# Kernel tuning notes

Hardware: AMD Instinct MI355X
Metric: run time of the kernel (lower is better)

Reference implementation:

```python
import jax, jax.numpy as jnp
import numpy as np

SEQ, BATCH, IN_DIM, HID, OUT = 512, 256, 300, 256, 2


def setup_inputs() -> dict:
    key = jax.random.key(0)
    ks = jax.random.split(key, 7)
    s_ih = 1.0 / np.sqrt(HID)
    return {
        "x": jax.random.normal(ks[0], (SEQ, BATCH, IN_DIM), jnp.float32),
        "W_ih": jax.random.uniform(ks[1], (HID, IN_DIM), jnp.float32, -s_ih, s_ih),
        "W_hh": jax.random.uniform(ks[2], (HID, HID), jnp.float32, -s_ih, s_ih),
        "b_ih": jax.random.uniform(ks[3], (HID,), jnp.float32, -s_ih, s_ih),
        "b_hh": jax.random.uniform(ks[4], (HID,), jnp.float32, -s_ih, s_ih),
        "W_fc": jax.random.uniform(ks[5], (OUT, HID), jnp.float32, -s_ih, s_ih),
        "b_fc": jax.random.uniform(ks[6], (OUT,), jnp.float32, -s_ih, s_ih),
    }


def reference(x, W_ih, W_hh, b_ih, b_hh, W_fc, b_fc):
    # Precompute input projection for all timesteps at once: [T, B, H]
    xp = jnp.einsum('tbi,hi->tbh', x, W_ih) + b_ih + b_hh

    def step(h, xt):
        h_new = jnp.tanh(xt + h @ W_hh.T)
        return h_new, None

    h0 = jnp.zeros((x.shape[1], W_hh.shape[0]), x.dtype)
    hT, _ = jax.lax.scan(step, h0, xp)  # hT: [B, H]
    # Dropout(0.3) is identity in eval mode.
    logits = hT @ W_fc.T + b_fc  # [B, 2]
    return jax.nn.log_softmax(logits, axis=-1)
```

## Files before the change

### kernel.cpp

```cpp
#include <hip/hip_runtime.h>
#include <hip/hip_bf16.h>
#include <cstdint>
#include <cstddef>

#define SEQ 512
#define BATCH 256
#define IN_DIM 300
#define HID 256

typedef __attribute__((ext_vector_type(8))) short bf16x8;
typedef __attribute__((ext_vector_type(4))) float f32x4;

__device__ __forceinline__ unsigned short f2bf(float f) {
  union { float f; unsigned int u; } v; v.f = f;
  unsigned int u = v.u;
  return (unsigned short)((u + 0x7fffu + ((u >> 16) & 1u)) >> 16);
}
__device__ __forceinline__ unsigned short f2bf_fast(float f) {
  union { float f; unsigned int u; } v; v.f = f;
  return (unsigned short)((v.u + 0x8000u) >> 16);
}
__device__ __forceinline__ float bitsf(unsigned int u) {
  union { unsigned int u; float f; } v; v.u = u; return v.f;
}
__device__ __forceinline__ bf16x8 cvt8(float a0,float a1,float a2,float a3,
                                       float a4,float a5,float a6,float a7) {
  union { __hip_bfloat162 h2[4]; bf16x8 v; } c;
  c.h2[0] = __float22bfloat162_rn(make_float2(a0, a1));
  c.h2[1] = __float22bfloat162_rn(make_float2(a2, a3));
  c.h2[2] = __float22bfloat162_rn(make_float2(a4, a5));
  c.h2[3] = __float22bfloat162_rn(make_float2(a6, a7));
  return c.v;
}

__global__ __launch_bounds__(256) void conv_wih(const float* __restrict__ w,
                                                unsigned short* __restrict__ w_bf) {
  int idx = blockIdx.x * 256 + threadIdx.x;
  int n = idx / 320, k = idx - n * 320;
  float v = (k < IN_DIM) ? w[n * IN_DIM + k] : 0.f;
  w_bf[idx] = f2bf(v);
}

__global__ __launch_bounds__(256) void gemm_xp(const float* __restrict__ x,
    const unsigned short* __restrict__ w_bf, const float* __restrict__ b_ih,
    const float* __restrict__ b_hh, unsigned int* __restrict__ xp2)
{
  __shared__ unsigned short a_lds[64][40];
  __shared__ unsigned short w_lds[256][40];
  const int tid  = threadIdx.x;
  const int wave = tid >> 6;
  const int lane = tid & 63;
  const int l15  = lane & 15;
  const int quad = lane >> 4;
  const long m0 = (long)blockIdx.x * 64;

  f32x4 acc[4][4];
  #pragma unroll
  for (int mt = 0; mt < 4; ++mt)
    #pragma unroll
    for (int nt = 0; nt < 4; ++nt) acc[mt][nt] = (f32x4){0.f, 0.f, 0.f, 0.f};

  const int ar = tid >> 2;
  const int ac = (tid & 3) * 8;

  float av[8];
  uint2 wv[8];
  {
    const float* src = x + (size_t)(m0 + ar) * IN_DIM + ac;
    float2 p0 = *(const float2*)(src + 0);
    float2 p1 = *(const float2*)(src + 2);
    float2 p2 = *(const float2*)(src + 4);
    float2 p3 = *(const float2*)(src + 6);
    av[0]=p0.x; av[1]=p0.y; av[2]=p1.x; av[3]=p1.y;
    av[4]=p2.x; av[5]=p2.y; av[6]=p3.x; av[7]=p3.y;
    #pragma unroll
    for (int i = 0; i < 8; ++i) {
      int e = tid + i * 256;
      wv[i] = *(const uint2*)(w_bf + (e >> 3) * 320 + (e & 7) * 4);
    }
  }

  for (int kc = 0; kc < 10; ++kc) {
    *(bf16x8*)&a_lds[ar][ac] = cvt8(av[0],av[1],av[2],av[3],av[4],av[5],av[6],av[7]);
    #pragma unroll
    for (int i = 0; i < 8; ++i) {
      int e = tid + i * 256;
      *(uint2*)&w_lds[e >> 3][(e & 7) * 4] = wv[i];
    }
    __syncthreads();
    if (kc < 9) {
      const int k0 = (kc + 1) * 32;
      const float* src = x + (size_t)(m0 + ar) * IN_DIM + (k0 + ac);
      if (k0 + ac + 8 <= IN_DIM) {
        float2 p0 = *(const float2*)(src + 0);
        float2 p1 = *(const float2*)(src + 2);
        float2 p2 = *(const float2*)(src + 4);
        float2 p3 = *(const float2*)(src + 6);
        av[0]=p0.x; av[1]=p0.y; av[2]=p1.x; av[3]=p1.y;
        av[4]=p2.x; av[5]=p2.y; av[6]=p3.x; av[7]=p3.y;
      } else {
        #pragma unroll
        for (int j = 0; j < 8; ++j) av[j] = (k0 + ac + j < IN_DIM) ? src[j] : 0.f;
      }
      #pragma unroll
      for (int i = 0; i < 8; ++i) {
        int e = tid + i * 256;
        wv[i] = *(const uint2*)(w_bf + (e >> 3) * 320 + k0 + (e & 7) * 4);
      }
    }
    bf16x8 afr[4], bfr[4];
    #pragma unroll
    for (int mt = 0; mt < 4; ++mt)
      afr[mt] = *(const bf16x8*)&a_lds[mt*16 + l15][quad*8];
    #pragma unroll
    for (int nt = 0; nt < 4; ++nt)
      bfr[nt] = *(const bf16x8*)&w_lds[wave*64 + nt*16 + l15][quad*8];
    #pragma unroll
    for (int mt = 0; mt < 4; ++mt)
      #pragma unroll
      for (int nt = 0; nt < 4; ++nt)
        acc[mt][nt] = __builtin_amdgcn_mfma_f32_16x16x32_bf16(afr[mt], bfr[nt], acc[mt][nt], 0, 0, 0);
    __syncthreads();
  }
  const int t = (int)(blockIdx.x >> 2);
  #pragma unroll
  for (int nt = 0; nt < 4; ++nt) {
    const int n = wave*64 + nt*16 + l15;
    const float kb = 2.0f * (b_ih[n] + b_hh[n]);
    const int tid_lo = (wave*2 + (nt>>1))*64 + (nt&1)*16 + l15;
    #pragma unroll
    for (int mt = 0; mt < 4; ++mt) {
      const int g = ((int)(blockIdx.x & 3))*16 + mt*4 + quad;
      const size_t base = ((size_t)t*64 + g)*512;
      float y0 = fmaf(2.0f, acc[mt][nt][0], kb);
      float y1 = fmaf(2.0f, acc[mt][nt][1], kb);
      float y2 = fmaf(2.0f, acc[mt][nt][2], kb);
      float y3 = fmaf(2.0f, acc[mt][nt][3], kb);
      union { __hip_bfloat162 h2; unsigned int u; } p01, p23;
      p01.h2 = __float22bfloat162_rn(make_float2(y0, y1));
      p23.h2 = __float22bfloat162_rn(make_float2(y2, y3));
      xp2[base + tid_lo]      = p01.u;
      xp2[base + tid_lo + 32] = p23.u;
    }
  }
}

__global__ __launch_bounds__(512) void rnn_scan(const float* __restrict__ W_hh,
    const unsigned int* __restrict__ xp2, float* __restrict__ hT)
{
  __shared__ alignas(16) unsigned short hbuf[2][4 * 272];
  const int tid  = threadIdx.x;
  const int wave = tid >> 6;
  const int lane = tid & 63;
  const int l15  = lane & 15;
  const int quad = lane >> 4;
  const int g = blockIdx.x;
  const int c0 = wave * 32;

  bf16x8 wf[2][8];
  #pragma unroll
  for (int nt = 0; nt < 2; ++nt) {
    const int n = c0 + nt*16 + l15;
    #pragma unroll
    for (int kc = 0; kc < 8; ++kc) {
      const float* src = W_hh + n*HID + kc*32 + quad*8;
      float4 p0 = *(const float4*)src;
      float4 p1 = *(const float4*)(src + 4);
      wf[nt][kc] = cvt8(p0.x,p0.y,p0.z,p0.w,p1.x,p1.y,p1.z,p1.w);
    }
  }

  const int rb    = (quad >> 1) * 2;
  const int col_e = c0 + (quad & 1) * 16 + l15;
  const int abase = (l15 & 3) * 272 + quad * 8;

  for (int i = tid; i < 4 * 272; i += 512) hbuf[0][i] = 0;

  const unsigned int* xbase = xp2 + (size_t)g * 512 + tid;

  __syncthreads();

  unsigned int xq[16];
  for (int tc = 0; tc < SEQ / 16; ++tc) {
    const unsigned int* pb = xbase + (size_t)tc * 16 * 32768;
    #pragma unroll
    for (int j = 0; j < 16; ++j)
      xq[j] = pb[(size_t)j * 32768];
    #pragma unroll
    for (int j = 0; j < 16; ++j) {
      const int cur = j & 1;
      bf16x8 afr[8];
      #pragma unroll
      for (int kc = 0; kc < 8; ++kc)
        afr[kc] = *(const bf16x8*)&hbuf[cur][abase + kc*32];
      f32x4 a0A = (f32x4){0.f,0.f,0.f,0.f}, a0B = a0A, a1A = a0A, a1B = a0A;
      #pragma unroll
      for (int kc = 0; kc < 8; kc += 2) {
        a0A = __builtin_amdgcn_mfma_f32_16x16x32_bf16(afr[kc],   wf[0][kc],   a0A, 0, 0, 0);
        a1A = __builtin_amdgcn_mfma_f32_16x16x32_bf16(afr[kc],   wf[1][kc],   a1A, 0, 0, 0);
        a0B = __builtin_amdgcn_mfma_f32_16x16x32_bf16(afr[kc+1], wf[0][kc+1], a0B, 0, 0, 0);
        a1B = __builtin_amdgcn_mfma_f32_16x16x32_bf16(afr[kc+1], wf[1][kc+1], a1B, 0, 0, 0);
      }
      f32x4 acc0 = a0A + a0B;
      f32x4 acc1 = a1A + a1B;
      f32x4 a = (quad & 1) ? acc1 : acc0;
      float s0 = (quad >> 1) ? a[2] : a[0];
      float s1 = (quad >> 1) ? a[3] : a[1];
      float xv0 = bitsf(xq[j] << 16);
      float xv1 = bitsf(xq[j] & 0xffff0000u);
      float y0 = fmaf(2.0f, s0, xv0);
      float y1 = fmaf(2.0f, s1, xv1);
      float h0 = fmaf(-2.0f, __builtin_amdgcn_rcpf(__expf(y0) + 1.0f), 1.0f);
      float h1 = fmaf(-2.0f, __builtin_amdgcn_rcpf(__expf(y1) + 1.0f), 1.0f);
      if (j < 15 || tc < SEQ/16 - 1) {
        hbuf[1 - cur][ rb      * 272 + col_e] = f2bf_fast(h0);
        hbuf[1 - cur][(rb + 1) * 272 + col_e] = f2bf_fast(h1);
      } else {
        hT[(size_t)(g*4 + rb    ) * HID + col_e] = h0;
        hT[(size_t)(g*4 + rb + 1) * HID + col_e] = h1;
      }
      __syncthreads();
    }
  }
}

__global__ __launch_bounds__(64) void fc_head(const float* __restrict__ hT,
    const float* __restrict__ W_fc, const float* __restrict__ b_fc,
    float* __restrict__ out)
{
  const int b = blockIdx.x;
  const int l = threadIdx.x;
  float s0 = 0.f, s1 = 0.f;
  #pragma unroll
  for (int j0 = 0; j0 < HID; j0 += 64) {
    float h = hT[(size_t)b * HID + j0 + l];
    s0 += h * W_fc[j0 + l];
    s1 += h * W_fc[HID + j0 + l];
  }
  #pragma unroll
  for (int off = 32; off > 0; off >>= 1) {
    s0 += __shfl_xor(s0, off, 64);
    s1 += __shfl_xor(s1, off, 64);
  }
  if (l == 0) {
    float l0 = s0 + b_fc[0], l1 = s1 + b_fc[1];
    float m = fmaxf(l0, l1);
    float lse = m + logf(expf(l0 - m) + expf(l1 - m));
    out[b*2 + 0] = l0 - lse;
    out[b*2 + 1] = l1 - lse;
  }
}

extern "C" void kernel_launch(void* const* d_in, const int* in_sizes, int n_in,
                              void* d_out, int out_size, void* d_ws, size_t ws_size,
                              hipStream_t stream) {
  const float* x    = (const float*)d_in[0];
  const float* W_ih = (const float*)d_in[1];
  const float* W_hh = (const float*)d_in[2];
  const float* b_ih = (const float*)d_in[3];
  const float* b_hh = (const float*)d_in[4];
  const float* W_fc = (const float*)d_in[5];
  const float* b_fc = (const float*)d_in[6];
  float* out = (float*)d_out;

  const size_t xp_bytes = (size_t)SEQ * BATCH * HID * 2;
  const size_t wb_bytes = (size_t)256 * 320 * 2;
  const size_t ht_bytes = (size_t)BATCH * HID * 4;
  if (ws_size < xp_bytes + wb_bytes + ht_bytes) return;

  char* ws = (char*)d_ws;
  unsigned int*   xp2  = (unsigned int*)ws;
  unsigned short* w_bf = (unsigned short*)(ws + xp_bytes);
  float*          hT   = (float*)(ws + xp_bytes + wb_bytes);

  hipLaunchKernelGGL(conv_wih, dim3(320),  dim3(256), 0, stream, W_ih, w_bf);
  hipLaunchKernelGGL(gemm_xp,  dim3(2048), dim3(256), 0, stream, x, w_bf, b_ih, b_hh, xp2);
  hipLaunchKernelGGL(rnn_scan, dim3(64),   dim3(512), 0, stream, W_hh, xp2, hT);
  hipLaunchKernelGGL(fc_head,  dim3(BATCH), dim3(64), 0, stream, hT, W_fc, b_fc, out);
}
```

Measured before the change: 500.8 us.

## Keep W_ih in registers in GEMM and prefetch next xp chunk in scan

The input-projection GEMM now uses 512-thread blocks over 128 rows. Each wave holds its 32-column slice of W_ih as bf16 fragments in registers, which removes the per-k-chunk W staging through LDS and leaves only the x tile in shared memory. The recurrent scan prefetches the next 16 timesteps of projected input into a second register set while computing the current chunk, hiding global load latency on the serial critical path. Both kernels replace __syncthreads with a barrier that only waits on LDS counters. This raises register pressure and could lower occupancy.

```diff
diff --git a/kernel.cpp b/kernel.cpp
--- a/kernel.cpp
+++ b/kernel.cpp
@@ -10,6 +10,7 @@
 
 typedef __attribute__((ext_vector_type(8))) short bf16x8;
 typedef __attribute__((ext_vector_type(4))) float f32x4;
+typedef __attribute__((ext_vector_type(4))) unsigned int u32x4;
 
 __device__ __forceinline__ unsigned short f2bf(float f) {
   union { float f; unsigned int u; } v; v.f = f;
@@ -22,6 +23,11 @@
 }
 __device__ __forceinline__ float bitsf(unsigned int u) {
   union { unsigned int u; float f; } v; v.u = u; return v.f;
+}
+__device__ __forceinline__ unsigned int cvtpk(float lo, float hi) {
+  union { __hip_bfloat162 h; unsigned int u; } c;
+  c.h = __float22bfloat162_rn(make_float2(lo, hi));
+  return c.u;
 }
 __device__ __forceinline__ bf16x8 cvt8(float a0,float a1,float a2,float a3,
                                        float a4,float a5,float a6,float a7) {
@@ -32,6 +38,11 @@
   c.h2[3] = __float22bfloat162_rn(make_float2(a6, a7));
   return c.v;
 }
+__device__ __forceinline__ void barrier_lgkm() {
+  asm volatile("s_waitcnt lgkmcnt(0)" ::: "memory");
+  __builtin_amdgcn_s_barrier();
+  asm volatile("" ::: "memory");
+}
 
 __global__ __launch_bounds__(256) void conv_wih(const float* __restrict__ w,
                                                 unsigned short* __restrict__ w_bf) {
@@ -41,56 +52,60 @@
   w_bf[idx] = f2bf(v);
 }
 
-__global__ __launch_bounds__(256) void gemm_xp(const float* __restrict__ x,
+__global__ __launch_bounds__(512) void gemm_xp(const float* __restrict__ x,
     const unsigned short* __restrict__ w_bf, const float* __restrict__ b_ih,
     const float* __restrict__ b_hh, unsigned int* __restrict__ xp2)
 {
-  __shared__ unsigned short a_lds[64][40];
-  __shared__ unsigned short w_lds[256][40];
+  __shared__ unsigned int a_lds[128][20];
   const int tid  = threadIdx.x;
   const int wave = tid >> 6;
   const int lane = tid & 63;
   const int l15  = lane & 15;
   const int quad = lane >> 4;
-  const long m0 = (long)blockIdx.x * 64;
-
-  f32x4 acc[4][4];
-  #pragma unroll
-  for (int mt = 0; mt < 4; ++mt)
-    #pragma unroll
-    for (int nt = 0; nt < 4; ++nt) acc[mt][nt] = (f32x4){0.f, 0.f, 0.f, 0.f};
+  const long m0  = (long)blockIdx.x * 128;
+
+  bf16x8 wf[2][10];
+  #pragma unroll
+  for (int nt = 0; nt < 2; ++nt) {
+    const unsigned short* wp = w_bf + (size_t)(wave*32 + nt*16 + l15) * 320 + quad*8;
+    #pragma unroll
+    for (int kc = 0; kc < 10; ++kc)
+      wf[nt][kc] = *(const bf16x8*)(wp + kc*32);
+  }
+
+  f32x4 acc[8][2];
+  #pragma unroll
+  for (int mt = 0; mt < 8; ++mt) {
+    acc[mt][0] = (f32x4){0.f, 0.f, 0.f, 0.f};
+    acc[mt][1] = (f32x4){0.f, 0.f, 0.f, 0.f};
+  }
 
   const int ar = tid >> 2;
   const int ac = (tid & 3) * 8;
+  const float* xrow = x + (size_t)(m0 + ar) * IN_DIM;
 
   float av[8];
-  uint2 wv[8];
   {
-    const float* src = x + (size_t)(m0 + ar) * IN_DIM + ac;
-    float2 p0 = *(const float2*)(src + 0);
-    float2 p1 = *(const float2*)(src + 2);
-    float2 p2 = *(const float2*)(src + 4);
-    float2 p3 = *(const float2*)(src + 6);
+    float2 p0 = *(const float2*)(xrow + ac + 0);
+    float2 p1 = *(const float2*)(xrow + ac + 2);
+    float2 p2 = *(const float2*)(xrow + ac + 4);
+    float2 p3 = *(const float2*)(xrow + ac + 6);
     av[0]=p0.x; av[1]=p0.y; av[2]=p1.x; av[3]=p1.y;
     av[4]=p2.x; av[5]=p2.y; av[6]=p3.x; av[7]=p3.y;
-    #pragma unroll
-    for (int i = 0; i < 8; ++i) {
-      int e = tid + i * 256;
-      wv[i] = *(const uint2*)(w_bf + (e >> 3) * 320 + (e & 7) * 4);
-    }
-  }
-
+  }
+
+  #pragma unroll
   for (int kc = 0; kc < 10; ++kc) {
-    *(bf16x8*)&a_lds[ar][ac] = cvt8(av[0],av[1],av[2],av[3],av[4],av[5],av[6],av[7]);
-    #pragma unroll
-    for (int i = 0; i < 8; ++i) {
-      int e = tid + i * 256;
-      *(uint2*)&w_lds[e >> 3][(e & 7) * 4] = wv[i];
-    }
-    __syncthreads();
+    u32x4 pk;
+    pk.x = cvtpk(av[0], av[1]);
+    pk.y = cvtpk(av[2], av[3]);
+    pk.z = cvtpk(av[4], av[5]);
+    pk.w = cvtpk(av[6], av[7]);
+    *(u32x4*)&a_lds[ar][(tid & 3) * 4] = pk;
+    barrier_lgkm();
     if (kc < 9) {
       const int k0 = (kc + 1) * 32;
-      const float* src = x + (size_t)(m0 + ar) * IN_DIM + (k0 + ac);
+      const float* src = xrow + k0 + ac;
       if (k0 + ac + 8 <= IN_DIM) {
         float2 p0 = *(const float2*)(src + 0);
         float2 p1 = *(const float2*)(src + 2);
@@ -102,45 +117,33 @@
         #pragma unroll
         for (int j = 0; j < 8; ++j) av[j] = (k0 + ac + j < IN_DIM) ? src[j] : 0.f;
       }
-      #pragma unroll
-      for (int i = 0; i < 8; ++i) {
-        int e = tid + i * 256;
-        wv[i] = *(const uint2*)(w_bf + (e >> 3) * 320 + k0 + (e & 7) * 4);
-      }
-    }
-    bf16x8 afr[4], bfr[4];
-    #pragma unroll
-    for (int mt = 0; mt < 4; ++mt)
-      afr[mt] = *(const bf16x8*)&a_lds[mt*16 + l15][quad*8];
-    #pragma unroll
-    for (int nt = 0; nt < 4; ++nt)
-      bfr[nt] = *(const bf16x8*)&w_lds[wave*64 + nt*16 + l15][quad*8];
-    #pragma unroll
-    for (int mt = 0; mt < 4; ++mt)
-      #pragma unroll
-      for (int nt = 0; nt < 4; ++nt)
-        acc[mt][nt] = __builtin_amdgcn_mfma_f32_16x16x32_bf16(afr[mt], bfr[nt], acc[mt][nt], 0, 0, 0);
-    __syncthreads();
-  }
-  const int t = (int)(blockIdx.x >> 2);
-  #pragma unroll
-  for (int nt = 0; nt < 4; ++nt) {
-    const int n = wave*64 + nt*16 + l15;
+    }
+    #pragma unroll
+    for (int mt = 0; mt < 8; ++mt) {
+      bf16x8 afr = *(const bf16x8*)&a_lds[mt*16 + l15][quad*4];
+      acc[mt][0] = __builtin_amdgcn_mfma_f32_16x16x32_bf16(afr, wf[0][kc], acc[mt][0], 0, 0, 0);
+      acc[mt][1] = __builtin_amdgcn_mfma_f32_16x16x32_bf16(afr, wf[1][kc], acc[mt][1], 0, 0, 0);
+    }
+    barrier_lgkm();
+  }
+
+  const int t  = (int)(blockIdx.x >> 1);
+  const int b4 = ((int)blockIdx.x & 1) * 32;
+  #pragma unroll
+  for (int nt = 0; nt < 2; ++nt) {
+    const int n = wave*32 + nt*16 + l15;
     const float kb = 2.0f * (b_ih[n] + b_hh[n]);
-    const int tid_lo = (wave*2 + (nt>>1))*64 + (nt&1)*16 + l15;
-    #pragma unroll
-    for (int mt = 0; mt < 4; ++mt) {
-      const int g = ((int)(blockIdx.x & 3))*16 + mt*4 + quad;
-      const size_t base = ((size_t)t*64 + g)*512;
+    const int tid_lo = wave*64 + nt*16 + l15;
+    #pragma unroll
+    for (int mt = 0; mt < 8; ++mt) {
+      const int g = b4 + mt*4 + quad;
+      const size_t base = ((size_t)t*64 + g) * 512;
       float y0 = fmaf(2.0f, acc[mt][nt][0], kb);
       float y1 = fmaf(2.0f, acc[mt][nt][1], kb);
       float y2 = fmaf(2.0f, acc[mt][nt][2], kb);
       float y3 = fmaf(2.0f, acc[mt][nt][3], kb);
-      union { __hip_bfloat162 h2; unsigned int u; } p01, p23;
-      p01.h2 = __float22bfloat162_rn(make_float2(y0, y1));
-      p23.h2 = __float22bfloat162_rn(make_float2(y2, y3));
-      xp2[base + tid_lo]      = p01.u;
-      xp2[base + tid_lo + 32] = p23.u;
+      xp2[base + tid_lo]      = cvtpk(y0, y1);
+      xp2[base + tid_lo + 32] = cvtpk(y2, y3);
     }
   }
 }
@@ -180,12 +183,18 @@
 
   __syncthreads();
 
-  unsigned int xq[16];
+  unsigned int xq[16], xqn[16];
+  #pragma unroll
+  for (int j = 0; j < 16; ++j)
+    xq[j] = xbase[(size_t)j * 32768];
+
   for (int tc = 0; tc < SEQ / 16; ++tc) {
-    const unsigned int* pb = xbase + (size_t)tc * 16 * 32768;
-    #pragma unroll
-    for (int j = 0; j < 16; ++j)
-      xq[j] = pb[(size_t)j * 32768];
+    if (tc < SEQ/16 - 1) {
+      const unsigned int* pn = xbase + (size_t)(tc + 1) * 16 * 32768;
+      #pragma unroll
+      for (int j = 0; j < 16; ++j)
+        xqn[j] = pn[(size_t)j * 32768];
+    }
     #pragma unroll
     for (int j = 0; j < 16; ++j) {
       const int cur = j & 1;
@@ -219,7 +228,12 @@
         hT[(size_t)(g*4 + rb    ) * HID + col_e] = h0;
         hT[(size_t)(g*4 + rb + 1) * HID + col_e] = h1;
       }
-      __syncthreads();
+      barrier_lgkm();
+    }
+    if (tc < SEQ/16 - 1) {
+      #pragma unroll
+      for (int j = 0; j < 16; ++j)
+        xq[j] = xqn[j];
     }
   }
 }
@@ -274,7 +288,7 @@
   float*          hT   = (float*)(ws + xp_bytes + wb_bytes);
 
   hipLaunchKernelGGL(conv_wih, dim3(320),  dim3(256), 0, stream, W_ih, w_bf);
-  hipLaunchKernelGGL(gemm_xp,  dim3(2048), dim3(256), 0, stream, x, w_bf, b_ih, b_hh, xp2);
+  hipLaunchKernelGGL(gemm_xp,  dim3(1024), dim3(512), 0, stream, x, w_bf, b_ih, b_hh, xp2);
   hipLaunchKernelGGL(rnn_scan, dim3(64),   dim3(512), 0, stream, W_hh, xp2, hT);
   hipLaunchKernelGGL(fc_head,  dim3(BATCH), dim3(64), 0, stream, hT, W_fc, b_fc, out);
 }
```

Result: no change. 492.5 us (-1.7%).
